# Performance work log

Hardware: AMD Instinct MI355X
Metric: run time of the kernel (lower is better)

## Reference

```python
import jax, jax.numpy as jnp
import numpy as np

C = 256
G = min(C // 4, 32)  # GroupNorm groups = 32
EPS = 1e-6


def group_norm(x, gamma, beta):
    B, Cc, H, W = x.shape
    xg = x.reshape(B, G, Cc // G, H, W)
    mean = xg.mean(axis=(2, 3, 4), keepdims=True)
    var = xg.var(axis=(2, 3, 4), keepdims=True)
    xg = (xg - mean) / jnp.sqrt(var + EPS)
    x = xg.reshape(B, Cc, H, W)
    return x * gamma[None, :, None, None] + beta[None, :, None, None]


def nin(h, W_, b_):
    # 1x1 conv as channel contraction: [B,C,H,W] x [C,D] -> [B,D,H,W]
    return jnp.einsum('bchw,cd->bdhw', h, W_) + b_[None, :, None, None]


def setup_inputs() -> dict:
    key = jax.random.key(0)
    ks = jax.random.split(key, 12)
    B, H, Wd = 4, 64, 64
    x = jax.random.normal(ks[0], (B, C, H, Wd), dtype=jnp.float32)
    gn_gamma = jnp.ones((C,), jnp.float32)
    gn_beta = jnp.zeros((C,), jnp.float32)
    scale = 0.1
    w0 = jax.random.normal(ks[1], (C, C), jnp.float32) * scale
    b0 = jnp.zeros((C,), jnp.float32)
    w1 = jax.random.normal(ks[2], (C, C), jnp.float32) * scale
    b1 = jnp.zeros((C,), jnp.float32)
    w2 = jax.random.normal(ks[3], (C, C), jnp.float32) * scale
    b2 = jnp.zeros((C,), jnp.float32)
    w3 = jax.random.normal(ks[4], (C, C), jnp.float32) * scale
    b3 = jnp.zeros((C,), jnp.float32)
    return {"x": x, "gn_gamma": gn_gamma, "gn_beta": gn_beta,
            "w0": w0, "b0": b0, "w1": w1, "b1": b1,
            "w2": w2, "b2": b2, "w3": w3, "b3": b3}


def reference(x, gn_gamma, gn_beta, w0, b0, w1, b1, w2, b2, w3, b3):
    B, Cc, H, Wd = x.shape
    h = group_norm(x, gn_gamma, gn_beta)
    q = nin(h, w0, b0)
    k = nin(h, w1, b1)
    v = nin(h, w2, b2)
    # attention over all spatial positions; scores [B,H,W,H,W]
    w = jnp.einsum('bchw,bcij->bhwij', q, k) * (Cc ** -0.5)
    w = jax.nn.softmax(w.reshape(B, H, Wd, H * Wd), axis=-1)
    w = w.reshape(B, H, Wd, H, Wd)
    h = jnp.einsum('bhwij,bcij->bchw', w, v)
    h = nin(h, w3, b3)
    return x + h  # skip_rescale=False
```

## Files before the change

kernel.cpp:

```cpp
#include <hip/hip_runtime.h>
#include <math.h>


typedef short short8    __attribute__((ext_vector_type(8)));
typedef ushort ushort8  __attribute__((ext_vector_type(8)));
typedef ushort ushort4v __attribute__((ext_vector_type(4)));
typedef float f32x4     __attribute__((ext_vector_type(4)));
typedef float f32x16    __attribute__((ext_vector_type(16)));

#define BB 4
#define CCH 256
#define NSP 4096
#define TEN ((size_t)BB * NSP * CCH)

__device__ __forceinline__ float b2f(ushort h){
  unsigned int u = ((unsigned int)h) << 16;
  float f; __builtin_memcpy(&f, &u, 4); return f;
}
__device__ __forceinline__ ushort f2b(float f){
  unsigned int u; __builtin_memcpy(&u, &f, 4);
  u += 0x7fffu + ((u >> 16) & 1u);
  return (ushort)(u >> 16);
}
__device__ __forceinline__ unsigned int pk2(float a, float b){
  unsigned int r;
  asm("v_cvt_pk_bf16_f32 %0, %1, %2" : "=&v"(r) : "v"(a), "v"(b));
  return r;
}

__global__ __launch_bounds__(256) void pre_k(const float* __restrict__ x,
                                             const float* __restrict__ w0,
                                             const float* __restrict__ w1,
                                             const float* __restrict__ w2,
                                             const float* __restrict__ w3,
                                             ushort* __restrict__ wT,
                                             float* __restrict__ sums){
  __shared__ ushort tile[64][72];
  __shared__ float red[8];
  const int bxx = blockIdx.x;
  const int t = threadIdx.x;
  if (bxx < 64){
    const int wsel = bxx >> 4, tb = bxx & 15;
    const float* w = (wsel==0) ? w0 : (wsel==1) ? w1 : (wsel==2) ? w2 : w3;
    ushort* dst = wT + (size_t)wsel * 65536;
    const int r0 = (tb >> 2) * 64, c0 = (tb & 3) * 64;
    #pragma unroll
    for (int p = 0; p < 2; p++){
      const int r = p*32 + (t >> 3), cc = (t & 7)*8;
      const float* wr = w + (size_t)(r0 + r)*256 + c0 + cc;
      f32x4 a = *(const f32x4*)wr;
      f32x4 d = *(const f32x4*)(wr + 4);
      #pragma unroll
      for (int j = 0; j < 4; j++){
        tile[r][cc + j]     = f2b(a[j]);
        tile[r][cc + 4 + j] = f2b(d[j]);
      }
    }
    __syncthreads();
    #pragma unroll
    for (int p = 0; p < 2; p++){
      const int r = p*32 + (t >> 3), cc = (t & 7)*8;
      ushort8 ov;
      #pragma unroll
      for (int j = 0; j < 8; j++) ov[j] = tile[cc + j][r];
      *(ushort8*)(dst + (size_t)(c0 + r)*256 + r0 + cc) = ov;
    }
  } else {
    const int q = bxx - 64;
    const f32x4* p = (const f32x4*)(x + (size_t)(q >> 1)*32768 + (size_t)(q & 1)*16384);
    float s = 0.f, s2 = 0.f;
    for (int i = t; i < 4096; i += 256){
      f32x4 v = p[i];
      #pragma unroll
      for (int j = 0; j < 4; j++){ s += v[j]; s2 += v[j]*v[j]; }
    }
    #pragma unroll
    for (int off = 32; off >= 1; off >>= 1){
      s  += __shfl_down(s,  off, 64);
      s2 += __shfl_down(s2, off, 64);
    }
    const int w = t >> 6;
    if ((t & 63) == 0){ red[w*2] = s; red[w*2+1] = s2; }
    __syncthreads();
    if (t == 0){
      sums[q*2]   = red[0]+red[2]+red[4]+red[6];
      sums[q*2+1] = red[1]+red[3]+red[5]+red[7];
    }
  }
}

__global__ __launch_bounds__(256) void gn_apply_k(const float* __restrict__ x,
                                                  const float* __restrict__ sums,
                                                  const float* __restrict__ gamma,
                                                  const float* __restrict__ beta,
                                                  ushort* __restrict__ h_t){
  __shared__ ushort tile[64][72];
  const int b = blockIdx.z, c0 = blockIdx.y*64, n0 = blockIdx.x*64;
  const int t = threadIdx.x;
  #pragma unroll
  for (int p = 0; p < 2; p++){
    const int cl = p*32 + (t >> 3);
    const int nc = (t & 7) * 8;
    const int c = c0 + cl;
    const int bg = b*32 + (c>>3);
    const float S  = sums[bg*4+0] + sums[bg*4+2];
    const float S2 = sums[bg*4+1] + sums[bg*4+3];
    const float mean = S * (1.f/32768.f);
    const float rstd = rsqrtf(fmaxf(S2*(1.f/32768.f) - mean*mean, 0.f) + 1e-6f);
    const float sc = rstd * gamma[c];
    const float sh = beta[c] - mean * sc;
    const float* xr = x + ((size_t)b*CCH + c)*NSP + n0 + nc;
    f32x4 a = *(const f32x4*)xr;
    f32x4 d = *(const f32x4*)(xr + 4);
    #pragma unroll
    for (int j = 0; j < 4; j++){
      tile[nc + j][cl]     = f2b(a[j]*sc + sh);
      tile[nc + 4 + j][cl] = f2b(d[j]*sc + sh);
    }
  }
  __syncthreads();
  #pragma unroll
  for (int p = 0; p < 2; p++){
    const int nl = p*32 + (t >> 3);
    const int cc = (t & 7) * 8;
    ushort8 ov;
    #pragma unroll
    for (int j = 0; j < 8; j++) ov[j] = tile[nl][cc + j];
    *(ushort8*)(h_t + ((size_t)b*NSP + n0 + nl)*CCH + c0 + cc) = ov;
  }
}

__global__ __launch_bounds__(256) void gemm_qkv_k(const ushort* __restrict__ wT,
                                                  const ushort* __restrict__ h_t,
                                                  ushort* __restrict__ q_t,
                                                  ushort* __restrict__ k_t,
                                                  ushort* __restrict__ vout,
                                                  const float* __restrict__ b0,
                                                  const float* __restrict__ b1,
                                                  const float* __restrict__ b2){
  __shared__ ushort Bt[64*256];
  const int K = 256;
  const long HS = (long)NSP * CCH;
  const int t = threadIdx.x, w = t >> 6, lane = t & 63;
  const int li = lane & 15, quad = lane >> 4;
  const int batch = blockIdx.y;

  if (blockIdx.z == 0){
    const ushort* Bm = h_t + (size_t)batch * HS;
    ushort* out0 = q_t + (size_t)batch * HS;
    ushort* out1 = k_t + (size_t)batch * HS;
    const int nb = blockIdx.x * 64;

    #pragma unroll
    for (int i = 0; i < 8; i++){
      const int id = t + 256*i;
      const int row = id >> 5, gg = id & 31;
      *(ushort8*)&Bt[row*256 + (gg ^ (row & 31))*8] =
        *(const ushort8*)(Bm + (size_t)(nb + row)*K + gg*8);
    }
    __syncthreads();

    for (int tm = 0; tm < 4; tm++){
      const int m0 = tm*64 + w*16;
      short8 afr0[8], afr1[8];
      #pragma unroll
      for (int kk = 0; kk < 8; kk++){
        afr0[kk] = *(const short8*)(wT +         (size_t)(m0 + li)*K + kk*32 + quad*8);
        afr1[kk] = *(const short8*)(wT + 65536 + (size_t)(m0 + li)*K + kk*32 + quad*8);
      }
      #pragma unroll
      for (int nt = 0; nt < 4; nt++){
        f32x4 acc0 = {0.f,0.f,0.f,0.f};
        f32x4 acc1 = {0.f,0.f,0.f,0.f};
        const int n = nb + nt*16 + li;
        const int rowl = nt*16 + li;
        #pragma unroll
        for (int kk = 0; kk < 8; kk++){
          short8 bfr = *(const short8*)&Bt[rowl*256 + ((4*kk + quad) ^ (rowl & 31))*8];
          acc0 = __builtin_amdgcn_mfma_f32_16x16x32_bf16(afr0[kk], bfr, acc0, 0, 0, 0);
          acc1 = __builtin_amdgcn_mfma_f32_16x16x32_bf16(afr1[kk], bfr, acc1, 0, 0, 0);
        }
        float e0[4], e1[4];
        #pragma unroll
        for (int r2 = 0; r2 < 4; r2++){
          e0[r2] = acc0[r2] + b0[m0 + quad*4 + r2];
          e1[r2] = acc1[r2] + b1[m0 + quad*4 + r2];
        }
        uint2 d0; d0.x = pk2(e0[0], e0[1]); d0.y = pk2(e0[2], e0[3]);
        uint2 d1; d1.x = pk2(e1[0], e1[1]); d1.y = pk2(e1[2], e1[3]);
        *(uint2*)(out0 + (size_t)n*256 + m0 + quad*4) = d0;
        *(uint2*)(out1 + (size_t)n*256 + m0 + quad*4) = d1;
      }
    }
  } else {
    const ushort* A  = h_t + (size_t)batch * HS;
    const ushort* Bm = wT + 2*65536;
    ushort* OutT = vout + (size_t)batch * HS;
    const int m0 = blockIdx.x*64 + w*16;

    short8 afr[8];
    #pragma unroll
    for (int kk = 0; kk < 8; kk++)
      afr[kk] = *(const short8*)(A + (size_t)(m0 + li)*K + kk*32 + quad*8);

    for (int tn = 0; tn < 4; tn++){
      const int nb = tn*64;
      __syncthreads();
      #pragma unroll
      for (int i = 0; i < 8; i++){
        const int id = t + 256*i;
        const int row = id >> 5, gg = id & 31;
        *(ushort8*)&Bt[row*256 + (gg ^ (row & 31))*8] =
          *(const ushort8*)(Bm + (size_t)(nb + row)*K + gg*8);
      }
      __syncthreads();

      #pragma unroll
      for (int nt = 0; nt < 4; nt++){
        f32x4 acc = {0.f,0.f,0.f,0.f};
        const int n = nb + nt*16 + li;
        const int rowl = nt*16 + li;
        #pragma unroll
        for (int kk = 0; kk < 8; kk++){
          short8 bfr = *(const short8*)&Bt[rowl*256 + ((4*kk + quad) ^ (rowl & 31))*8];
          acc = __builtin_amdgcn_mfma_f32_16x16x32_bf16(afr[kk], bfr, acc, 0, 0, 0);
        }
        const float bn = b2[n];
        float e[4];
        #pragma unroll
        for (int r2 = 0; r2 < 4; r2++) e[r2] = acc[r2] + bn;
        uint2 dv; dv.x = pk2(e[0], e[1]); dv.y = pk2(e[2], e[3]);
        *(uint2*)(OutT + (size_t)n*4096 + m0 + quad*4) = dv;
      }
    }
  }
}

__global__ __launch_bounds__(256, 2) void attn32_k(const ushort* __restrict__ qg,
                                                   const ushort* __restrict__ kg,
                                                   const ushort* __restrict__ vg,
                                                   ushort* __restrict__ ph01,
                                                   ushort* __restrict__ ph23,
                                                   float* __restrict__ lbuf,
                                                   int iters, int ks4){
  __shared__ ushort Kt[32*260];
  __shared__ ushort Vt[256*36];

  const int t = threadIdx.x, lane = t & 63;
  const int cl = lane & 31, h = lane >> 5;
  const int bx = blockIdx.x;
  const int qt = bx / ks4;
  const int r  = bx % ks4;
  const int s  = r >> 2, b = r & 3;
  const int n0 = qt * 128;
  const int w = t >> 6;
  const int qb = n0 + w*32;
  const int keybase = s * (iters * 32);

  const ushort* kb = kg + (size_t)b*NSP*CCH;
  const ushort* vb = vg + (size_t)b*CCH*NSP;

  short8 qf[16];
  {
    const ushort* qrow = qg + ((size_t)b*NSP + qb + cl)*CCH + h*8;
    #pragma unroll
    for (int st = 0; st < 16; st++) qf[st] = *(const short8*)(qrow + st*16);
  }

  f32x16 oacc[8];
  #pragma unroll
  for (int i = 0; i < 8; i++) oacc[i] = (f32x16)(0.f);
  float l_i = 0.f;
  const float c1 = 0.0625f * 1.44269504088896f;
  const float M2 = 24.f;

  ushort8 kreg[4];
  #pragma unroll
  for (int i = 0; i < 4; i++){
    const int id = t + 256*i;
    kreg[i] = *(const ushort8*)(kb + (size_t)(keybase + (id>>5))*CCH + (id&31)*8);
  }

  for (int it = 0; it < iters; it++){
    const int key0 = keybase + it*32;
    __syncthreads();
    ushort8 vreg[4];
    #pragma unroll
    for (int i = 0; i < 4; i++){
      const int id = t + 256*i;
      vreg[i] = *(const ushort8*)(vb + (size_t)(id>>2)*NSP + key0 + (id&3)*8);
    }
    #pragma unroll
    for (int i = 0; i < 4; i++){
      const int id = t + 256*i;
      *(ushort8*)&Kt[(id>>5)*260 + (id&31)*8] = kreg[i];
    }
    #pragma unroll
    for (int i = 0; i < 4; i++){
      const int id = t + 256*i;
      *(ushort8*)&Vt[(id>>2)*36 + (id&3)*8] = vreg[i];
    }
    __syncthreads();

    if (it + 1 < iters){
      const int nk0 = key0 + 32;
      #pragma unroll
      for (int i = 0; i < 4; i++){
        const int id = t + 256*i;
        kreg[i] = *(const ushort8*)(kb + (size_t)(nk0 + (id>>5))*CCH + (id&31)*8);
      }
    }

    f32x16 sacc = (f32x16)(0.f);
    #pragma unroll
    for (int st = 0; st < 16; st++){
      short8 kf = *(const short8*)&Kt[cl*260 + st*16 + h*8];
      sacc = __builtin_amdgcn_mfma_f32_32x32x16_bf16(kf, qf[st], sacc, 0, 0, 0);
    }

    unsigned int grp[4][2];
    #pragma unroll
    for (int m = 0; m < 4; m++){
      float p0 = __builtin_amdgcn_exp2f(fminf(sacc[4*m+0]*c1 - M2, 30.f));
      float p1 = __builtin_amdgcn_exp2f(fminf(sacc[4*m+1]*c1 - M2, 30.f));
      float p2 = __builtin_amdgcn_exp2f(fminf(sacc[4*m+2]*c1 - M2, 30.f));
      float p3 = __builtin_amdgcn_exp2f(fminf(sacc[4*m+3]*c1 - M2, 30.f));
      l_i += (p0 + p1) + (p2 + p3);
      grp[m][0] = pk2(p0, p1);
      grp[m][1] = pk2(p2, p3);
    }
    unsigned int sa0 = h ? grp[0][0] : grp[1][0];
    unsigned int sa1 = h ? grp[0][1] : grp[1][1];
    unsigned int sb0 = h ? grp[2][0] : grp[3][0];
    unsigned int sb1 = h ? grp[2][1] : grp[3][1];
    unsigned int ra0 = __shfl_xor((int)sa0, 32, 64);
    unsigned int ra1 = __shfl_xor((int)sa1, 32, 64);
    unsigned int rb0 = __shfl_xor((int)sb0, 32, 64);
    unsigned int rb1 = __shfl_xor((int)sb1, 32, 64);
    unsigned int f0[4], f1[4];
    if (h == 0){
      f0[0]=grp[0][0]; f0[1]=grp[0][1]; f0[2]=ra0; f0[3]=ra1;
      f1[0]=grp[2][0]; f1[1]=grp[2][1]; f1[2]=rb0; f1[3]=rb1;
    } else {
      f0[0]=ra0; f0[1]=ra1; f0[2]=grp[1][0]; f0[3]=grp[1][1];
      f1[0]=rb0; f1[1]=rb1; f1[2]=grp[3][0]; f1[3]=grp[3][1];
    }
    short8 pf0, pf1;
    __builtin_memcpy(&pf0, f0, 16);
    __builtin_memcpy(&pf1, f1, 16);

    #pragma unroll
    for (int ct = 0; ct < 8; ct++){
      short8 v0 = *(const short8*)&Vt[(ct*32 + cl)*36 + h*8];
      short8 v1 = *(const short8*)&Vt[(ct*32 + cl)*36 + 16 + h*8];
      oacc[ct] = __builtin_amdgcn_mfma_f32_32x32x16_bf16(pf0, v0, oacc[ct], 0, 0, 0);
      oacc[ct] = __builtin_amdgcn_mfma_f32_32x32x16_bf16(pf1, v1, oacc[ct], 0, 0, 0);
    }
  }

  ushort* ps = (s < 2) ? (ph01 + (size_t)s*TEN) : (ph23 + (size_t)(s-2)*TEN);
  ps += (size_t)b * NSP * CCH;
  #pragma unroll
  for (int ct = 0; ct < 8; ct++){
    const size_t crow = (size_t)(ct*32 + cl) * NSP;
    #pragma unroll
    for (int m = 0; m < 4; m++){
      unsigned int d0 = pk2(oacc[ct][4*m+0], oacc[ct][4*m+1]);
      unsigned int d1 = pk2(oacc[ct][4*m+2], oacc[ct][4*m+3]);
      uint2 dv; dv.x = d0; dv.y = d1;
      *(uint2*)(ps + crow + qb + 8*m + 4*h) = dv;
    }
  }
  l_i += __shfl_xor(l_i, 32, 64);
  if (h == 0)
    lbuf[(size_t)s*BB*NSP + (size_t)b*NSP + qb + cl] = l_i;
}

__global__ __launch_bounds__(256) void combine_k(const ushort* __restrict__ ph01,
                                                 const ushort* __restrict__ ph23,
                                                 const float* __restrict__ lbuf,
                                                 ushort* __restrict__ Oc, int ks){
  __shared__ ushort T[64*66];
  const int t = threadIdx.x;
  const int q0 = blockIdx.x * 64, c0 = blockIdx.y * 64, b = blockIdx.z;
  const int ql4 = (t & 15) * 4;
  const int cs  = t >> 4;
  float rl[4];
  #pragma unroll
  for (int j = 0; j < 4; j++){
    float suml = 0.f;
    for (int sp = 0; sp < ks; sp++)
      suml += lbuf[(size_t)sp*BB*NSP + (size_t)b*NSP + q0 + ql4 + j];
    rl[j] = 1.f / suml;
  }
  #pragma unroll
  for (int ci = 0; ci < 4; ci++){
    const int c = cs*4 + ci;
    float acc[4] = {0.f, 0.f, 0.f, 0.f};
    for (int sp = 0; sp < ks; sp++){
      const ushort* pp = (sp < 2) ? (ph01 + (size_t)sp*TEN) : (ph23 + (size_t)(sp-2)*TEN);
      ushort4v u = *(const ushort4v*)(pp + ((size_t)b*CCH + c0 + c)*NSP + q0 + ql4);
      #pragma unroll
      for (int j = 0; j < 4; j++) acc[j] += b2f(u[j]);
    }
    #pragma unroll
    for (int j = 0; j < 4; j++)
      T[(ql4 + j)*66 + c] = f2b(acc[j] * rl[j]);
  }
  __syncthreads();
  const int q2 = t >> 2, ch = (t & 3) * 16;
  ushort8 o0, o1;
  #pragma unroll
  for (int j = 0; j < 8; j++){ o0[j] = T[q2*66 + ch + j]; o1[j] = T[q2*66 + ch + 8 + j]; }
  ushort* dst = Oc + ((size_t)b*NSP + q0 + q2)*CCH + c0 + ch;
  *(ushort8*)dst = o0;
  *(ushort8*)(dst + 8) = o1;
}

__global__ __launch_bounds__(256) void gemm_proj_k(const ushort* __restrict__ A,
                                                   const ushort* __restrict__ Bm,
                                                   const float* __restrict__ b3,
                                                   const float* __restrict__ xin,
                                                   float* __restrict__ out){
  __shared__ ushort Bt[64*256];
  const int K = 256;
  const int t = threadIdx.x, w = t >> 6, lane = t & 63;
  const int li = lane & 15, quad = lane >> 4;
  const int tm = blockIdx.x & 63, tn = blockIdx.x >> 6;
  const int batch = blockIdx.y;
  A   += (size_t)batch * NSP * CCH;
  xin += (size_t)batch * CCH * NSP;
  out += (size_t)batch * CCH * NSP;
  const int m0 = tm*64 + w*16;
  const int nb = tn*64;

  #pragma unroll
  for (int i = 0; i < 8; i++){
    const int id = t + 256*i;
    const int row = id >> 5, gg = id & 31;
    *(ushort8*)&Bt[row*256 + (gg ^ (row & 31))*8] =
      *(const ushort8*)(Bm + (size_t)(nb + row)*K + gg*8);
  }
  short8 afr[8];
  #pragma unroll
  for (int kk = 0; kk < 8; kk++)
    afr[kk] = *(const short8*)(A + (size_t)(m0 + li)*K + kk*32 + quad*8);
  __syncthreads();

  #pragma unroll
  for (int nt = 0; nt < 4; nt++){
    f32x4 acc = {0.f,0.f,0.f,0.f};
    const int d = nb + nt*16 + li;
    const int rowl = nt*16 + li;
    #pragma unroll
    for (int kk = 0; kk < 8; kk++){
      short8 bfr = *(const short8*)&Bt[rowl*256 + ((4*kk + quad) ^ (rowl & 31))*8];
      acc = __builtin_amdgcn_mfma_f32_16x16x32_bf16(afr[kk], bfr, acc, 0, 0, 0);
    }
    const float bias = b3[d];
    const size_t idx = (size_t)d*NSP + m0 + quad*4;
    f32x4 xv = *(const f32x4*)(xin + idx);
    f32x4 ov;
    #pragma unroll
    for (int r = 0; r < 4; r++) ov[r] = acc[r] + bias + xv[r];
    *(f32x4*)(out + idx) = ov;
  }
}

extern "C" void kernel_launch(void* const* d_in, const int* in_sizes, int n_in,
                              void* d_out, int out_size, void* d_ws, size_t ws_size,
                              hipStream_t stream){
  const float* x     = (const float*)d_in[0];
  const float* gamma = (const float*)d_in[1];
  const float* beta  = (const float*)d_in[2];
  const float* w0    = (const float*)d_in[3];
  const float* b0    = (const float*)d_in[4];
  const float* w1    = (const float*)d_in[5];
  const float* b1    = (const float*)d_in[6];
  const float* w2    = (const float*)d_in[7];
  const float* b2    = (const float*)d_in[8];
  const float* w3    = (const float*)d_in[9];
  const float* b3    = (const float*)d_in[10];
  float* out = (float*)d_out;

  ushort* h_t  = (ushort*)d_out;
  ushort* ph01 = (ushort*)d_out;
  ushort* q_t = (ushort*)d_ws;
  ushort* k_t = q_t + TEN;
  ushort* v   = k_t + TEN;
  ushort* wT  = v + TEN;
  float* sums  = (float*)(wT + 4*65536);
  float* lbuf  = sums + 512;
  ushort* ph23 = (ushort*)(lbuf + 4*BB*NSP);

  const size_t need4 = ((3*TEN + 4*65536)*2) + (512 + 4*BB*NSP)*4 + 2*TEN*2;
  const int ks = (ws_size >= need4) ? 4 : 2;
  const int iters = NSP / (ks * 32);

  pre_k<<<dim3(320), 256, 0, stream>>>(x, w0, w1, w2, w3, wT, sums);
  gn_apply_k<<<dim3(64,4,4), 256, 0, stream>>>(x, sums, gamma, beta, h_t);
  gemm_qkv_k<<<dim3(64, BB, 2), 256, 0, stream>>>(wT, h_t, q_t, k_t, v, b0, b1, b2);

  attn32_k<<<128*ks, 256, 0, stream>>>(q_t, k_t, v, ph01, ph23, lbuf, iters, 4*ks);

  ushort* Oc = k_t;
  combine_k<<<dim3(64, 4, BB), 256, 0, stream>>>(ph01, ph23, lbuf, Oc, ks);
  gemm_proj_k<<<dim3(256, BB), 256, 0, stream>>>(Oc, wT + 3*65536, b3, x, out);
}
```

Measured before the change: 242.4 us.

## Fuse GroupNorm apply into QKV projection GEMM via shared-memory normalized tile

Merges the GroupNorm apply kernel and the QKV GEMM into one kernel. Each block normalizes a 32-position slice of x straight into a swizzled LDS tile and uses it as the operand for the Q, K and V projections. This removes the bf16 h_t round trip through global memory and one kernel launch. In exchange each block now stages all four chunks of the V weight into LDS, where before two z-halves split the work, and uses more shared memory.

Result: no change. 244.4 us (+0.9%).

```diff
diff --git a/kernel.cpp b/kernel.cpp
--- a/kernel.cpp
+++ b/kernel.cpp
@@ -89,20 +89,31 @@
   }
 }
 
-__global__ __launch_bounds__(256) void gn_apply_k(const float* __restrict__ x,
-                                                  const float* __restrict__ sums,
-                                                  const float* __restrict__ gamma,
-                                                  const float* __restrict__ beta,
-                                                  ushort* __restrict__ h_t){
-  __shared__ ushort tile[64][72];
-  const int b = blockIdx.z, c0 = blockIdx.y*64, n0 = blockIdx.x*64;
-  const int t = threadIdx.x;
-  #pragma unroll
-  for (int p = 0; p < 2; p++){
-    const int cl = p*32 + (t >> 3);
-    const int nc = (t & 7) * 8;
-    const int c = c0 + cl;
-    const int bg = b*32 + (c>>3);
+__global__ __launch_bounds__(256) void gn_qkv_k(const float* __restrict__ x,
+                                                const float* __restrict__ sums,
+                                                const float* __restrict__ gamma,
+                                                const float* __restrict__ beta,
+                                                const ushort* __restrict__ wT,
+                                                ushort* __restrict__ q_t,
+                                                ushort* __restrict__ k_t,
+                                                ushort* __restrict__ vout,
+                                                const float* __restrict__ b0,
+                                                const float* __restrict__ b1,
+                                                const float* __restrict__ b2){
+  __shared__ ushort Hs[32*256];
+  __shared__ ushort Bt[64*256];
+  const int K = 256;
+  const long HS = (long)NSP * CCH;
+  const int t = threadIdx.x, w = t >> 6, lane = t & 63;
+  const int li = lane & 15, quad = lane >> 4;
+  const int b = blockIdx.y;
+  const int n0 = blockIdx.x * 32;
+
+  #pragma unroll
+  for (int p = 0; p < 4; p++){
+    const int c = p*64 + (t >> 2);
+    const int nc = (t & 3) * 8;
+    const int bg = b*32 + (c >> 3);
     const float S  = sums[bg*4+0] + sums[bg*4+2];
     const float S2 = sums[bg*4+1] + sums[bg*4+3];
     const float mean = S * (1.f/32768.f);
@@ -112,126 +123,87 @@
     const float* xr = x + ((size_t)b*CCH + c)*NSP + n0 + nc;
     f32x4 a = *(const f32x4*)xr;
     f32x4 d = *(const f32x4*)(xr + 4);
+    const int gg = c >> 3, co = c & 7;
     #pragma unroll
     for (int j = 0; j < 4; j++){
-      tile[nc + j][cl]     = f2b(a[j]*sc + sh);
-      tile[nc + 4 + j][cl] = f2b(d[j]*sc + sh);
+      const int n1 = nc + j, n2 = nc + 4 + j;
+      Hs[n1*256 + ((gg ^ n1) & 31)*8 + co] = f2b(a[j]*sc + sh);
+      Hs[n2*256 + ((gg ^ n2) & 31)*8 + co] = f2b(d[j]*sc + sh);
     }
   }
   __syncthreads();
-  #pragma unroll
-  for (int p = 0; p < 2; p++){
-    const int nl = p*32 + (t >> 3);
-    const int cc = (t & 7) * 8;
-    ushort8 ov;
-    #pragma unroll
-    for (int j = 0; j < 8; j++) ov[j] = tile[nl][cc + j];
-    *(ushort8*)(h_t + ((size_t)b*NSP + n0 + nl)*CCH + c0 + cc) = ov;
-  }
-}
-
-__global__ __launch_bounds__(256) void gemm_qkv_k(const ushort* __restrict__ wT,
-                                                  const ushort* __restrict__ h_t,
-                                                  ushort* __restrict__ q_t,
-                                                  ushort* __restrict__ k_t,
-                                                  ushort* __restrict__ vout,
-                                                  const float* __restrict__ b0,
-                                                  const float* __restrict__ b1,
-                                                  const float* __restrict__ b2){
-  __shared__ ushort Bt[64*256];
-  const int K = 256;
-  const long HS = (long)NSP * CCH;
-  const int t = threadIdx.x, w = t >> 6, lane = t & 63;
-  const int li = lane & 15, quad = lane >> 4;
-  const int batch = blockIdx.y;
-
-  if (blockIdx.z == 0){
-    const ushort* Bm = h_t + (size_t)batch * HS;
-    ushort* out0 = q_t + (size_t)batch * HS;
-    ushort* out1 = k_t + (size_t)batch * HS;
-    const int nb = blockIdx.x * 64;
-
+
+  ushort* out0 = q_t + (size_t)b * HS;
+  ushort* out1 = k_t + (size_t)b * HS;
+  for (int tm = 0; tm < 4; tm++){
+    const int m0 = tm*64 + w*16;
+    short8 afr0[8], afr1[8];
+    #pragma unroll
+    for (int kk = 0; kk < 8; kk++){
+      afr0[kk] = *(const short8*)(wT +         (size_t)(m0 + li)*K + kk*32 + quad*8);
+      afr1[kk] = *(const short8*)(wT + 65536 + (size_t)(m0 + li)*K + kk*32 + quad*8);
+    }
+    #pragma unroll
+    for (int nt = 0; nt < 2; nt++){
+      f32x4 acc0 = {0.f,0.f,0.f,0.f};
+      f32x4 acc1 = {0.f,0.f,0.f,0.f};
+      const int rowl = nt*16 + li;
+      const int n = n0 + rowl;
+      #pragma unroll
+      for (int kk = 0; kk < 8; kk++){
+        short8 bfr = *(const short8*)&Hs[rowl*256 + (((4*kk + quad) ^ rowl) & 31)*8];
+        acc0 = __builtin_amdgcn_mfma_f32_16x16x32_bf16(afr0[kk], bfr, acc0, 0, 0, 0);
+        acc1 = __builtin_amdgcn_mfma_f32_16x16x32_bf16(afr1[kk], bfr, acc1, 0, 0, 0);
+      }
+      float e0[4], e1[4];
+      #pragma unroll
+      for (int r2 = 0; r2 < 4; r2++){
+        e0[r2] = acc0[r2] + b0[m0 + quad*4 + r2];
+        e1[r2] = acc1[r2] + b1[m0 + quad*4 + r2];
+      }
+      uint2 d0; d0.x = pk2(e0[0], e0[1]); d0.y = pk2(e0[2], e0[3]);
+      uint2 d1; d1.x = pk2(e1[0], e1[1]); d1.y = pk2(e1[2], e1[3]);
+      *(uint2*)(out0 + (size_t)n*256 + m0 + quad*4) = d0;
+      *(uint2*)(out1 + (size_t)n*256 + m0 + quad*4) = d1;
+    }
+  }
+
+  ushort* OutT = vout + (size_t)b * HS;
+  const int arow = (w & 1)*16 + li;
+  const int m0v = n0 + (w & 1)*16;
+  short8 afr[8];
+  #pragma unroll
+  for (int kk = 0; kk < 8; kk++)
+    afr[kk] = *(const short8*)&Hs[arow*256 + (((4*kk + quad) ^ arow) & 31)*8];
+
+  const ushort* Bm = wT + 2*65536;
+  for (int tn = 0; tn < 4; tn++){
+    __syncthreads();
     #pragma unroll
     for (int i = 0; i < 8; i++){
       const int id = t + 256*i;
       const int row = id >> 5, gg = id & 31;
       *(ushort8*)&Bt[row*256 + (gg ^ (row & 31))*8] =
-        *(const ushort8*)(Bm + (size_t)(nb + row)*K + gg*8);
-    }
-    __syncthreads();
-
-    for (int tm = 0; tm < 4; tm++){
-      const int m0 = tm*64 + w*16;
-      short8 afr0[8], afr1[8];
+        *(const ushort8*)(Bm + (size_t)(tn*64 + row)*K + gg*8);
+    }
+    __syncthreads();
+
+    #pragma unroll
+    for (int s2i = 0; s2i < 2; s2i++){
+      f32x4 acc = {0.f,0.f,0.f,0.f};
+      const int rowb = (w >> 1)*32 + s2i*16 + li;
+      const int d = tn*64 + rowb;
       #pragma unroll
       for (int kk = 0; kk < 8; kk++){
-        afr0[kk] = *(const short8*)(wT +         (size_t)(m0 + li)*K + kk*32 + quad*8);
-        afr1[kk] = *(const short8*)(wT + 65536 + (size_t)(m0 + li)*K + kk*32 + quad*8);
+        short8 bfr = *(const short8*)&Bt[rowb*256 + (((4*kk + quad) ^ rowb) & 31)*8];
+        acc = __builtin_amdgcn_mfma_f32_16x16x32_bf16(afr[kk], bfr, acc, 0, 0, 0);
       }
-      #pragma unroll
-      for (int nt = 0; nt < 4; nt++){
-        f32x4 acc0 = {0.f,0.f,0.f,0.f};
-        f32x4 acc1 = {0.f,0.f,0.f,0.f};
-        const int n = nb + nt*16 + li;
-        const int rowl = nt*16 + li;
-        #pragma unroll
-        for (int kk = 0; kk < 8; kk++){
-          short8 bfr = *(const short8*)&Bt[rowl*256 + ((4*kk + quad) ^ (rowl & 31))*8];
-          acc0 = __builtin_amdgcn_mfma_f32_16x16x32_bf16(afr0[kk], bfr, acc0, 0, 0, 0);
-          acc1 = __builtin_amdgcn_mfma_f32_16x16x32_bf16(afr1[kk], bfr, acc1, 0, 0, 0);
-        }
-        float e0[4], e1[4];
-        #pragma unroll
-        for (int r2 = 0; r2 < 4; r2++){
-          e0[r2] = acc0[r2] + b0[m0 + quad*4 + r2];
-          e1[r2] = acc1[r2] + b1[m0 + quad*4 + r2];
-        }
-        uint2 d0; d0.x = pk2(e0[0], e0[1]); d0.y = pk2(e0[2], e0[3]);
-        uint2 d1; d1.x = pk2(e1[0], e1[1]); d1.y = pk2(e1[2], e1[3]);
-        *(uint2*)(out0 + (size_t)n*256 + m0 + quad*4) = d0;
-        *(uint2*)(out1 + (size_t)n*256 + m0 + quad*4) = d1;
-      }
-    }
-  } else {
-    const ushort* A  = h_t + (size_t)batch * HS;
-    const ushort* Bm = wT + 2*65536;
-    ushort* OutT = vout + (size_t)batch * HS;
-    const int m0 = blockIdx.x*64 + w*16;
-
-    short8 afr[8];
-    #pragma unroll
-    for (int kk = 0; kk < 8; kk++)
-      afr[kk] = *(const short8*)(A + (size_t)(m0 + li)*K + kk*32 + quad*8);
-
-    for (int tn = 0; tn < 4; tn++){
-      const int nb = tn*64;
-      __syncthreads();
-      #pragma unroll
-      for (int i = 0; i < 8; i++){
-        const int id = t + 256*i;
-        const int row = id >> 5, gg = id & 31;
-        *(ushort8*)&Bt[row*256 + (gg ^ (row & 31))*8] =
-          *(const ushort8*)(Bm + (size_t)(nb + row)*K + gg*8);
-      }
-      __syncthreads();
-
-      #pragma unroll
-      for (int nt = 0; nt < 4; nt++){
-        f32x4 acc = {0.f,0.f,0.f,0.f};
-        const int n = nb + nt*16 + li;
-        const int rowl = nt*16 + li;
-        #pragma unroll
-        for (int kk = 0; kk < 8; kk++){
-          short8 bfr = *(const short8*)&Bt[rowl*256 + ((4*kk + quad) ^ (rowl & 31))*8];
-          acc = __builtin_amdgcn_mfma_f32_16x16x32_bf16(afr[kk], bfr, acc, 0, 0, 0);
-        }
-        const float bn = b2[n];
-        float e[4];
-        #pragma unroll
-        for (int r2 = 0; r2 < 4; r2++) e[r2] = acc[r2] + bn;
-        uint2 dv; dv.x = pk2(e[0], e[1]); dv.y = pk2(e[2], e[3]);
-        *(uint2*)(OutT + (size_t)n*4096 + m0 + quad*4) = dv;
-      }
+      const float bn = b2[d];
+      float e[4];
+      #pragma unroll
+      for (int r2 = 0; r2 < 4; r2++) e[r2] = acc[r2] + bn;
+      uint2 dv; dv.x = pk2(e[0], e[1]); dv.y = pk2(e[2], e[3]);
+      *(uint2*)(OutT + (size_t)d*4096 + m0v + quad*4) = dv;
     }
   }
 }
@@ -483,7 +455,6 @@
   const float* b3    = (const float*)d_in[10];
   float* out = (float*)d_out;
 
-  ushort* h_t  = (ushort*)d_out;
   ushort* ph01 = (ushort*)d_out;
   ushort* q_t = (ushort*)d_ws;
   ushort* k_t = q_t + TEN;
@@ -498,8 +469,8 @@
   const int iters = NSP / (ks * 32);
 
   pre_k<<<dim3(320), 256, 0, stream>>>(x, w0, w1, w2, w3, wT, sums);
-  gn_apply_k<<<dim3(64,4,4), 256, 0, stream>>>(x, sums, gamma, beta, h_t);
-  gemm_qkv_k<<<dim3(64, BB, 2), 256, 0, stream>>>(wT, h_t, q_t, k_t, v, b0, b1, b2);
+  gn_qkv_k<<<dim3(128, BB), 256, 0, stream>>>(x, sums, gamma, beta, wT,
+                                              q_t, k_t, v, b0, b1, b2);
 
   attn32_k<<<128*ks, 256, 0, stream>>>(q_t, k_t, v, ph01, ph23, lbuf, iters, 4*ks);
 
```

## Double-buffer K/V tiles via direct global-to-LDS DMA in attention kernel

Applied to the files above, without the earlier changes.

Replaces register-staged K/V loads with global_load_lds transfers straight into shared memory, using two ping-pong LDS buffers. The next tile's copy is issued before the current tile's QK and PV MFMAs, so the load overlaps compute and one barrier per iteration is dropped. The LDS layout is reorganized into unpadded chunk-major form to match the 16-byte DMA granularity. The loop is now manually unrolled by two, which assumes an even iteration count. It also relies on the barrier correctly waiting for the asynchronous LDS writes, and it roughly doubles LDS use per block.

New measurement: 261.9 us. 8.1% more time.

```diff
diff --git a/kernel.cpp b/kernel.cpp
--- a/kernel.cpp
+++ b/kernel.cpp
@@ -26,6 +26,11 @@
   unsigned int r;
   asm("v_cvt_pk_bf16_f32 %0, %1, %2" : "=&v"(r) : "v"(a), "v"(b));
   return r;
+}
+__device__ __forceinline__ void dma16(const void* g, void* l){
+  __builtin_amdgcn_global_load_lds((const __attribute__((address_space(1))) void*)g,
+                                   (__attribute__((address_space(3))) void*)l,
+                                   16, 0, 0);
 }
 
 __global__ __launch_bounds__(256) void pre_k(const float* __restrict__ x,
@@ -236,6 +241,70 @@
   }
 }
 
+#define STAGE_KV(KDST, VDST, KEY0)                                              \
+  _Pragma("unroll")                                                             \
+  for (int i_ = 0; i_ < 4; i_++){                                               \
+    const int j_ = (w*4 + i_)*64 + lane;                                        \
+    dma16(kb + (size_t)((KEY0) + (j_ & 31))*CCH + (j_ >> 5)*8,                  \
+          &(KDST)[(w*4 + i_)*512]);                                             \
+    dma16(vb + (size_t)(j_ & 255)*NSP + (KEY0) + (j_ >> 8)*8,                   \
+          &(VDST)[(w*4 + i_)*512]);                                             \
+  }
+
+#define ATTN_STEP(KC, VC, KN, VN, IT)                                           \
+  {                                                                             \
+    const int it_ = (IT);                                                       \
+    const bool more_ = (it_ + 1 < iters);                                       \
+    if (more_){                                                                 \
+      const int nk0_ = keybase + (it_ + 1)*32;                                  \
+      STAGE_KV(KN, VN, nk0_);                                                   \
+    }                                                                           \
+    f32x16 sacc = (f32x16)(0.f);                                                \
+    _Pragma("unroll")                                                           \
+    for (int st = 0; st < 16; st++){                                            \
+      short8 kf = *(const short8*)&(KC)[((st*2 + h)*32 + cl)*8];                \
+      sacc = __builtin_amdgcn_mfma_f32_32x32x16_bf16(kf, qf[st], sacc, 0, 0, 0);\
+    }                                                                           \
+    unsigned int grp[4][2];                                                     \
+    _Pragma("unroll")                                                           \
+    for (int m = 0; m < 4; m++){                                                \
+      float p0 = __builtin_amdgcn_exp2f(fminf(sacc[4*m+0]*c1 - M2, 30.f));      \
+      float p1 = __builtin_amdgcn_exp2f(fminf(sacc[4*m+1]*c1 - M2, 30.f));      \
+      float p2 = __builtin_amdgcn_exp2f(fminf(sacc[4*m+2]*c1 - M2, 30.f));      \
+      float p3 = __builtin_amdgcn_exp2f(fminf(sacc[4*m+3]*c1 - M2, 30.f));      \
+      l_i += (p0 + p1) + (p2 + p3);                                             \
+      grp[m][0] = pk2(p0, p1);                                                  \
+      grp[m][1] = pk2(p2, p3);                                                  \
+    }                                                                           \
+    unsigned int sa0 = h ? grp[0][0] : grp[1][0];                               \
+    unsigned int sa1 = h ? grp[0][1] : grp[1][1];                               \
+    unsigned int sb0 = h ? grp[2][0] : grp[3][0];                               \
+    unsigned int sb1 = h ? grp[2][1] : grp[3][1];                               \
+    unsigned int ra0 = __shfl_xor((int)sa0, 32, 64);                            \
+    unsigned int ra1 = __shfl_xor((int)sa1, 32, 64);                            \
+    unsigned int rb0 = __shfl_xor((int)sb0, 32, 64);                            \
+    unsigned int rb1 = __shfl_xor((int)sb1, 32, 64);                            \
+    unsigned int f0[4], f1[4];                                                  \
+    if (h == 0){                                                                \
+      f0[0]=grp[0][0]; f0[1]=grp[0][1]; f0[2]=ra0; f0[3]=ra1;                   \
+      f1[0]=grp[2][0]; f1[1]=grp[2][1]; f1[2]=rb0; f1[3]=rb1;                   \
+    } else {                                                                    \
+      f0[0]=ra0; f0[1]=ra1; f0[2]=grp[1][0]; f0[3]=grp[1][1];                   \
+      f1[0]=rb0; f1[1]=rb1; f1[2]=grp[3][0]; f1[3]=grp[3][1];                   \
+    }                                                                           \
+    short8 pf0, pf1;                                                            \
+    __builtin_memcpy(&pf0, f0, 16);                                             \
+    __builtin_memcpy(&pf1, f1, 16);                                             \
+    _Pragma("unroll")                                                           \
+    for (int ct = 0; ct < 8; ct++){                                             \
+      short8 v0 = *(const short8*)&(VC)[(h*256 + ct*32 + cl)*8];                \
+      short8 v1 = *(const short8*)&(VC)[((2 + h)*256 + ct*32 + cl)*8];          \
+      oacc[ct] = __builtin_amdgcn_mfma_f32_32x32x16_bf16(pf0, v0, oacc[ct], 0, 0, 0); \
+      oacc[ct] = __builtin_amdgcn_mfma_f32_32x32x16_bf16(pf1, v1, oacc[ct], 0, 0, 0); \
+    }                                                                           \
+    if (more_) __syncthreads();                                                 \
+  }
+
 __global__ __launch_bounds__(256, 2) void attn32_k(const ushort* __restrict__ qg,
                                                    const ushort* __restrict__ kg,
                                                    const ushort* __restrict__ vg,
@@ -243,8 +312,8 @@
                                                    ushort* __restrict__ ph23,
                                                    float* __restrict__ lbuf,
                                                    int iters, int ks4){
-  __shared__ ushort Kt[32*260];
-  __shared__ ushort Vt[256*36];
+  __shared__ ushort KtA[8192], KtB[8192];
+  __shared__ ushort VtA[8192], VtB[8192];
 
   const int t = threadIdx.x, lane = t & 63;
   const int cl = lane & 31, h = lane >> 5;
@@ -274,88 +343,12 @@
   const float c1 = 0.0625f * 1.44269504088896f;
   const float M2 = 24.f;
 
-  ushort8 kreg[4];
-  #pragma unroll
-  for (int i = 0; i < 4; i++){
-    const int id = t + 256*i;
-    kreg[i] = *(const ushort8*)(kb + (size_t)(keybase + (id>>5))*CCH + (id&31)*8);
-  }
-
-  for (int it = 0; it < iters; it++){
-    const int key0 = keybase + it*32;
-    __syncthreads();
-    ushort8 vreg[4];
-    #pragma unroll
-    for (int i = 0; i < 4; i++){
-      const int id = t + 256*i;
-      vreg[i] = *(const ushort8*)(vb + (size_t)(id>>2)*NSP + key0 + (id&3)*8);
-    }
-    #pragma unroll
-    for (int i = 0; i < 4; i++){
-      const int id = t + 256*i;
-      *(ushort8*)&Kt[(id>>5)*260 + (id&31)*8] = kreg[i];
-    }
-    #pragma unroll
-    for (int i = 0; i < 4; i++){
-      const int id = t + 256*i;
-      *(ushort8*)&Vt[(id>>2)*36 + (id&3)*8] = vreg[i];
-    }
-    __syncthreads();
-
-    if (it + 1 < iters){
-      const int nk0 = key0 + 32;
-      #pragma unroll
-      for (int i = 0; i < 4; i++){
-        const int id = t + 256*i;
-        kreg[i] = *(const ushort8*)(kb + (size_t)(nk0 + (id>>5))*CCH + (id&31)*8);
-      }
-    }
-
-    f32x16 sacc = (f32x16)(0.f);
-    #pragma unroll
-    for (int st = 0; st < 16; st++){
-      short8 kf = *(const short8*)&Kt[cl*260 + st*16 + h*8];
-      sacc = __builtin_amdgcn_mfma_f32_32x32x16_bf16(kf, qf[st], sacc, 0, 0, 0);
-    }
-
-    unsigned int grp[4][2];
-    #pragma unroll
-    for (int m = 0; m < 4; m++){
-      float p0 = __builtin_amdgcn_exp2f(fminf(sacc[4*m+0]*c1 - M2, 30.f));
-      float p1 = __builtin_amdgcn_exp2f(fminf(sacc[4*m+1]*c1 - M2, 30.f));
-      float p2 = __builtin_amdgcn_exp2f(fminf(sacc[4*m+2]*c1 - M2, 30.f));
-      float p3 = __builtin_amdgcn_exp2f(fminf(sacc[4*m+3]*c1 - M2, 30.f));
-      l_i += (p0 + p1) + (p2 + p3);
-      grp[m][0] = pk2(p0, p1);
-      grp[m][1] = pk2(p2, p3);
-    }
-    unsigned int sa0 = h ? grp[0][0] : grp[1][0];
-    unsigned int sa1 = h ? grp[0][1] : grp[1][1];
-    unsigned int sb0 = h ? grp[2][0] : grp[3][0];
-    unsigned int sb1 = h ? grp[2][1] : grp[3][1];
-    unsigned int ra0 = __shfl_xor((int)sa0, 32, 64);
-    unsigned int ra1 = __shfl_xor((int)sa1, 32, 64);
-    unsigned int rb0 = __shfl_xor((int)sb0, 32, 64);
-    unsigned int rb1 = __shfl_xor((int)sb1, 32, 64);
-    unsigned int f0[4], f1[4];
-    if (h == 0){
-      f0[0]=grp[0][0]; f0[1]=grp[0][1]; f0[2]=ra0; f0[3]=ra1;
-      f1[0]=grp[2][0]; f1[1]=grp[2][1]; f1[2]=rb0; f1[3]=rb1;
-    } else {
-      f0[0]=ra0; f0[1]=ra1; f0[2]=grp[1][0]; f0[3]=grp[1][1];
-      f1[0]=rb0; f1[1]=rb1; f1[2]=grp[3][0]; f1[3]=grp[3][1];
-    }
-    short8 pf0, pf1;
-    __builtin_memcpy(&pf0, f0, 16);
-    __builtin_memcpy(&pf1, f1, 16);
-
-    #pragma unroll
-    for (int ct = 0; ct < 8; ct++){
-      short8 v0 = *(const short8*)&Vt[(ct*32 + cl)*36 + h*8];
-      short8 v1 = *(const short8*)&Vt[(ct*32 + cl)*36 + 16 + h*8];
-      oacc[ct] = __builtin_amdgcn_mfma_f32_32x32x16_bf16(pf0, v0, oacc[ct], 0, 0, 0);
-      oacc[ct] = __builtin_amdgcn_mfma_f32_32x32x16_bf16(pf1, v1, oacc[ct], 0, 0, 0);
-    }
+  STAGE_KV(KtA, VtA, keybase);
+  __syncthreads();
+
+  for (int it = 0; it < iters; it += 2){
+    ATTN_STEP(KtA, VtA, KtB, VtB, it);
+    ATTN_STEP(KtB, VtB, KtA, VtA, it + 1);
   }
 
   ushort* ps = (s < 2) ? (ph01 + (size_t)s*TEN) : (ph23 + (size_t)(s-2)*TEN);
```
